# Performance work log

Measured on AMD Instinct MI355X. Metric: run time of the kernel, lower is better.

Reference implementation:

```python
import jax, jax.numpy as jnp
import numpy as np

N_KERNELS = 5
MUL_FACTOR = 2.0
# 2.0 ** (arange(5) - 2) = [0.25, 0.5, 1, 2, 4]
BANDWIDTH_MULTIPLIERS = MUL_FACTOR ** (np.arange(N_KERNELS) - N_KERNELS // 2)


def setup_inputs() -> dict:
    key = jax.random.key(0)
    kx, ky = jax.random.split(key)
    X = jax.random.normal(kx, (4096, 256), dtype=jnp.float32)
    Y = jax.random.normal(ky, (4096, 256), dtype=jnp.float32)
    return {"X": X, "Y": Y}


def _pairwise_sq_dists(Z):
    # ||z_i - z_j||^2 via GEMM; clamp tiny negatives from roundoff.
    sq = jnp.sum(Z * Z, axis=-1)  # [2N]
    d2 = sq[:, None] + sq[None, :] - 2.0 * (Z @ Z.T)  # [2N, 2N]
    return jnp.maximum(d2, 0.0)


def reference(X, Y):
    n = X.shape[0]
    Z = jnp.concatenate([X, Y], axis=0)  # [2N, D]
    d2 = _pairwise_sq_dists(Z)  # [2N, 2N]
    n_samples = d2.shape[0]
    # bandwidth uses .data in torch -> detached
    bandwidth = jax.lax.stop_gradient(d2.sum()) / (n_samples ** 2 - n_samples)
    mults = jnp.asarray(BANDWIDTH_MULTIPLIERS, dtype=d2.dtype)  # [5]
    # K = sum_k exp(-d2 / (bandwidth * mult_k))
    K = jnp.exp(-d2[None, :, :] / (bandwidth * mults)[:, None, None]).sum(axis=0)
    XX = K[:n, :n].mean()
    XY = K[:n, n:].mean()
    YY = K[n:, n:].mean()
    return XX - 2.0 * XY + YY
```

## Files before the change

### kernel.cpp

```cpp
#include <hip/hip_runtime.h>
#include <math.h>


#define N_HALF 4096
#define DIM 256
#define M_TOT 8192
#define TILE 128
#define NT 64
#define NT_HALF 32
#define NCHUNK 512

typedef unsigned short ushort_t;
typedef __attribute__((ext_vector_type(8))) short short8;
typedef __attribute__((ext_vector_type(4))) float floatx4;

__device__ ushort_t g_zf[M_TOT * DIM];

__device__ __forceinline__ ushort_t f2bf(float f) {
    unsigned u = __float_as_uint(f);
    u += 0x7fffu + ((u >> 16) & 1u);
    return (ushort_t)(u >> 16);
}

__device__ __forceinline__ void gload_lds16(const ushort_t* g, ushort_t* l) {
    __builtin_amdgcn_global_load_lds(
        (const __attribute__((address_space(1))) void*)g,
        (__attribute__((address_space(3))) void*)l, 16, 0, 0);
}

__device__ __forceinline__ void stage_slice2(const ushort_t* gA, const ushort_t* gB,
                                             ushort_t* buf, int kk0,
                                             int wave, int lane) {
#pragma unroll
    for (int s = 0; s < 2; ++s) {
#pragma unroll
        for (int i = 0; i < 2; ++i) {
            const int c = wave * 2 + i;
            gload_lds16(gA + (size_t)c * 4096 + (kk0 + s) * 512 + lane * 8,
                        buf + s * 4096 + c * 512);
            gload_lds16(gB + (size_t)c * 4096 + (kk0 + s) * 512 + lane * 8,
                        buf + 8192 + s * 4096 + c * 512);
        }
    }
}

__device__ __forceinline__ void compute_kk(const ushort_t* lA, const ushort_t* lB,
                                           int a0, int b0, int laneoff,
                                           floatx4 (&accv)[4][4]) {
    short8 af[4], bf[4];
#pragma unroll
    for (int mi = 0; mi < 4; ++mi)
        af[mi] = *(const short8*)(lA + (a0 + mi) * 512 + laneoff);
#pragma unroll
    for (int ni = 0; ni < 4; ++ni)
        bf[ni] = *(const short8*)(lB + (b0 + ni) * 512 + laneoff);
#pragma unroll
    for (int mi = 0; mi < 4; ++mi)
#pragma unroll
        for (int ni = 0; ni < 4; ++ni)
            accv[mi][ni] = __builtin_amdgcn_mfma_f32_16x16x32_bf16(
                af[mi], bf[ni], accv[mi][ni], 0, 0, 0);
}

__global__ __launch_bounds__(256) void k_prep(const float* __restrict__ X,
                                              const float* __restrict__ Y,
                                              float* __restrict__ sq,
                                              float* __restrict__ colsum_r,
                                              float* __restrict__ Ssum_r) {
    __shared__ float cpart[4][256];
    __shared__ float spart[4];
    const int t = threadIdx.x, wave = t >> 6, lane = t & 63;
    const int row0 = blockIdx.x * 16 + wave * 4;
    const int kk = lane >> 3, q = (lane >> 1) & 3, j0 = (lane & 1) * 4;
    float c0 = 0.f, c1 = 0.f, c2 = 0.f, c3 = 0.f, ssum = 0.f;
#pragma unroll
    for (int i = 0; i < 4; ++i) {
        const int row = row0 + i;
        const float* p = (row < N_HALF) ? (X + (size_t)row * DIM)
                                        : (Y + (size_t)(row - N_HALF) * DIM);
        const float4 v = *((const float4*)p + lane);
        ushort4 hi;
        hi.x = f2bf(v.x); hi.y = f2bf(v.y); hi.z = f2bf(v.z); hi.w = f2bf(v.w);
        const int rb = row >> 4, m = row & 15;
        *(ushort4*)(g_zf + (size_t)rb * 4096 + kk * 512 + q * 128 + m * 8 + j0) = hi;
        c0 += v.x; c1 += v.y; c2 += v.z; c3 += v.w;
        float s = fmaf(v.x, v.x, fmaf(v.y, v.y, fmaf(v.z, v.z, v.w * v.w)));
#pragma unroll
        for (int off = 32; off > 0; off >>= 1) s += __shfl_xor(s, off);
        if (lane == 0) sq[row] = s;
        ssum += s;
    }
    float4 cp; cp.x = c0; cp.y = c1; cp.z = c2; cp.w = c3;
    *(float4*)&cpart[wave][lane * 4] = cp;
    if (lane == 0) spart[wave] = ssum;
    __syncthreads();
    const float cs = cpart[0][t] + cpart[1][t] + cpart[2][t] + cpart[3][t];
    const int rep = blockIdx.x & 7;
    atomicAdd(&colsum_r[rep * 256 + t], cs);
    if (t == 0) atomicAdd(&Ssum_r[rep], spart[0] + spart[1] + spart[2] + spart[3]);
}

__global__ __launch_bounds__(256) void k_bw(const float* __restrict__ colsum_r,
                                            const float* __restrict__ Ssum_r,
                                            float* __restrict__ c2out) {
    __shared__ double sred[4];
    const int t = threadIdx.x, lane = t & 63, wave = t >> 6;
    float csf = 0.f;
#pragma unroll
    for (int r = 0; r < 8; ++r) csf += colsum_r[r * 256 + t];
    double p = (double)csf * (double)csf;
#pragma unroll
    for (int off = 32; off > 0; off >>= 1) p += __shfl_xor(p, off);
    if (lane == 0) sred[wave] = p;
    __syncthreads();
    if (t == 0) {
        const double SS = sred[0] + sred[1] + sred[2] + sred[3];
        float Sf = 0.f;
#pragma unroll
        for (int r = 0; r < 8; ++r) Sf += Ssum_r[r];
        const double sum_d2 = 2.0 * (double)M_TOT * (double)Sf - 2.0 * SS;
        const double bw = sum_d2 / ((double)M_TOT * (double)M_TOT - (double)M_TOT);
        c2out[0] = (float)(1.4426950408889634 / (4.0 * bw));
    }
}

__global__ __launch_bounds__(256, 2) void k_gram(const float* __restrict__ sq,
                                                 const float* __restrict__ c2p,
                                                 double* __restrict__ acc,
                                                 unsigned* __restrict__ cnt,
                                                 float* __restrict__ out) {
    __shared__ __attribute__((aligned(16))) ushort_t lds[2][16384];
    __shared__ double redw[4][3];

    const int bid = (int)blockIdx.x;
    const int cc = (bid & 7) * 64 + (bid >> 3);
    const int nst = ((cc & 15) == 0) ? 5 : 4;
    const int f0 = cc * 4 + ((cc + 15) >> 4);

    const int t = threadIdx.x;
    const int lane = t & 63, wave = t >> 6;
    const int l15 = lane & 15, quad = lane >> 4;
    const int wrow = (wave >> 1) * 64, wcol = (wave & 1) * 64;
    const int a0 = (wave >> 1) * 4, b0 = (wave & 1) * 4;
    const int laneoff = quad * 128 + l15 * 8;

    const float c2 = c2p[0];
    const float twoc2 = 2.f * c2;

    int ti = (int)((129.0f - sqrtf(16641.0f - 8.0f * (float)f0)) * 0.5f);
    if (ti < 0) ti = 0; if (ti > NT - 1) ti = NT - 1;
    while (ti * NT - ti * (ti - 1) / 2 > f0) --ti;
    while ((ti + 1) * NT - (ti + 1) * ti / 2 <= f0) ++ti;
    int tj = ti + (f0 - (ti * NT - ti * (ti - 1) / 2));

    const ushort_t* cgA = g_zf + (size_t)ti * 8 * 4096;
    const ushort_t* cgB = g_zf + (size_t)tj * 8 * 4096;

    stage_slice2(cgA, cgB, lds[0], 0, wave, lane);
    __syncthreads();

    double lxx = 0.0, lxy = 0.0, lyy = 0.0;
    int cur = 0;

#pragma unroll 1
    for (int s = 0; s < nst; ++s) {
        int nti = ti, ntj = tj + 1;
        if (ntj == NT) { ++nti; ntj = nti; }
        const ushort_t* ngA = g_zf + (size_t)nti * 8 * 4096;
        const ushort_t* ngB = g_zf + (size_t)ntj * 8 * 4096;

        floatx4 accv[4][4];
#pragma unroll
        for (int mi = 0; mi < 4; ++mi)
#pragma unroll
            for (int ni = 0; ni < 4; ++ni) accv[mi][ni] = (floatx4)0.f;

#pragma unroll
        for (int kk2 = 0; kk2 < 4; ++kk2) {
            if (kk2 < 3)
                stage_slice2(cgA, cgB, lds[cur ^ 1], (kk2 + 1) * 2, wave, lane);
            else if (s < nst - 1)
                stage_slice2(ngA, ngB, lds[cur ^ 1], 0, wave, lane);
            compute_kk(lds[cur], lds[cur] + 8192, a0, b0, laneoff, accv);
            compute_kk(lds[cur] + 4096, lds[cur] + 8192 + 4096,
                       a0, b0, laneoff, accv);
            __syncthreads();
            cur ^= 1;
        }

        const int arow0 = ti * TILE, brow0 = tj * TILE;
        float nsj[4];
#pragma unroll
        for (int ni = 0; ni < 4; ++ni)
            nsj[ni] = -c2 * sq[brow0 + wcol + ni * 16 + l15];
        floatx4 nsi4[4];
#pragma unroll
        for (int mi = 0; mi < 4; ++mi) {
            const float4 sv = *(const float4*)&sq[arow0 + wrow + mi * 16 + quad * 4];
            nsi4[mi][0] = -c2 * sv.x; nsi4[mi][1] = -c2 * sv.y;
            nsi4[mi][2] = -c2 * sv.z; nsi4[mi][3] = -c2 * sv.w;
        }
        floatx4 sum4 = (floatx4)0.f;
#pragma unroll
        for (int mi = 0; mi < 4; ++mi) {
#pragma unroll
            for (int ni = 0; ni < 4; ++ni) {
                const floatx4 addv = nsi4[mi] + (floatx4)nsj[ni];
                floatx4 arg = twoc2 * accv[mi][ni] + addv;
                floatx4 tt;
#pragma unroll
                for (int r = 0; r < 4; ++r) tt[r] = exp2f(fminf(arg[r], 0.f));
                const floatx4 t2 = tt * tt, t4 = t2 * t2, t8 = t4 * t4, t16 = t8 * t8;
                sum4 += (tt + t2) + (t4 + t8) + t16;
            }
        }
        const float fsum = (sum4[0] + sum4[1]) + (sum4[2] + sum4[3]);
        const double contrib = ((ti == tj) ? 1.0 : 2.0) * (double)fsum;
        if (tj < NT_HALF)       lxx += contrib;
        else if (ti < NT_HALF)  lxy += contrib;
        else                    lyy += contrib;

        ti = nti; tj = ntj; cgA = ngA; cgB = ngB;
    }

#pragma unroll
    for (int off = 32; off > 0; off >>= 1) {
        lxx += __shfl_xor(lxx, off);
        lxy += __shfl_xor(lxy, off);
        lyy += __shfl_xor(lyy, off);
    }
    if (lane == 0) { redw[wave][0] = lxx; redw[wave][1] = lxy; redw[wave][2] = lyy; }
    __syncthreads();
    if (t == 0) {
        double sxx = 0.0, sxy = 0.0, syy = 0.0;
#pragma unroll
        for (int wv = 0; wv < 4; ++wv) {
            sxx += redw[wv][0]; sxy += redw[wv][1]; syy += redw[wv][2];
        }
        if (sxx != 0.0) atomicAdd(&acc[0], sxx);
        if (sxy != 0.0) atomicAdd(&acc[1], sxy);
        if (syy != 0.0) atomicAdd(&acc[2], syy);
        __threadfence();
        const unsigned old = atomicAdd(cnt, 1u);
        if (old == (0xAAAAAAAAu + (unsigned)(NCHUNK - 1)) ||
            old == (unsigned)(NCHUNK - 1)) {
            const double xx = atomicAdd(&acc[0], 0.0);
            const double xy = atomicAdd(&acc[1], 0.0);
            const double yy = atomicAdd(&acc[2], 0.0);
            out[0] = (float)((xx + yy - xy) *
                             (1.0 / ((double)N_HALF * (double)N_HALF)));
        }
    }
}

extern "C" void kernel_launch(void* const* d_in, const int* in_sizes, int n_in,
                              void* d_out, int out_size, void* d_ws, size_t ws_size,
                              hipStream_t stream) {
    const float* X = (const float*)d_in[0];
    const float* Y = (const float*)d_in[1];
    char* ws = (char*)d_ws;
    float* sq        = (float*)ws;
    float* colsum_r  = (float*)(ws + 32768);
    float* Ssum_r    = (float*)(ws + 40960);
    unsigned* cnt    = (unsigned*)(ws + 40992);
    double* acc      = (double*)(ws + 41000);
    float* c2ws      = (float*)(ws + 41024);
    float* out = (float*)d_out;

    hipLaunchKernelGGL(k_prep, dim3(512), dim3(256), 0, stream,
                       X, Y, sq, colsum_r, Ssum_r);
    hipLaunchKernelGGL(k_bw, dim3(1), dim3(256), 0, stream,
                       colsum_r, Ssum_r, c2ws);
    hipLaunchKernelGGL(k_gram, dim3(NCHUNK), dim3(256), 0, stream,
                       sq, c2ws, acc, cnt, out);
}
```

Before: 115.5 us.

## Deepen GEMM staging to 4-buffer ring with explicit vmcnt waits

Replaces the double-buffered LDS staging of two k-slices per step with a four-slot ring holding single k-slices, keeping three slices in flight ahead of compute. A single barrier per slice is now gated by explicit s_waitcnt vmcnt counts instead of a full __syncthreads. Fragment loads are issued before the next global-to-LDS prefetch, and the MFMA block runs with raised wave priority. The goal is to hide global load latency across tile boundaries and cut barrier stalls. The cost is hand-tuned wait counts that must exactly match the number of outstanding loads.

```diff
diff --git a/kernel.cpp b/kernel.cpp
--- a/kernel.cpp
+++ b/kernel.cpp
@@ -28,38 +28,14 @@
         (__attribute__((address_space(3))) void*)l, 16, 0, 0);
 }
 
-__device__ __forceinline__ void stage_slice2(const ushort_t* gA, const ushort_t* gB,
-                                             ushort_t* buf, int kk0,
-                                             int wave, int lane) {
-#pragma unroll
-    for (int s = 0; s < 2; ++s) {
-#pragma unroll
-        for (int i = 0; i < 2; ++i) {
-            const int c = wave * 2 + i;
-            gload_lds16(gA + (size_t)c * 4096 + (kk0 + s) * 512 + lane * 8,
-                        buf + s * 4096 + c * 512);
-            gload_lds16(gB + (size_t)c * 4096 + (kk0 + s) * 512 + lane * 8,
-                        buf + 8192 + s * 4096 + c * 512);
-        }
-    }
-}
-
-__device__ __forceinline__ void compute_kk(const ushort_t* lA, const ushort_t* lB,
-                                           int a0, int b0, int laneoff,
-                                           floatx4 (&accv)[4][4]) {
-    short8 af[4], bf[4];
-#pragma unroll
-    for (int mi = 0; mi < 4; ++mi)
-        af[mi] = *(const short8*)(lA + (a0 + mi) * 512 + laneoff);
-#pragma unroll
-    for (int ni = 0; ni < 4; ++ni)
-        bf[ni] = *(const short8*)(lB + (b0 + ni) * 512 + laneoff);
-#pragma unroll
-    for (int mi = 0; mi < 4; ++mi)
-#pragma unroll
-        for (int ni = 0; ni < 4; ++ni)
-            accv[mi][ni] = __builtin_amdgcn_mfma_f32_16x16x32_bf16(
-                af[mi], bf[ni], accv[mi][ni], 0, 0, 0);
+__device__ __forceinline__ void stage1(const ushort_t* gA, const ushort_t* gB,
+                                       int kk, ushort_t* buf, int wave, int lane) {
+#pragma unroll
+    for (int i = 0; i < 2; ++i) {
+        const int c = wave * 2 + i;
+        gload_lds16(gA + (size_t)c * 4096 + kk * 512 + lane * 8, buf + c * 512);
+        gload_lds16(gB + (size_t)c * 4096 + kk * 512 + lane * 8, buf + 4096 + c * 512);
+    }
 }
 
 __global__ __launch_bounds__(256) void k_prep(const float* __restrict__ X,
@@ -129,7 +105,7 @@
                                                  double* __restrict__ acc,
                                                  unsigned* __restrict__ cnt,
                                                  float* __restrict__ out) {
-    __shared__ __attribute__((aligned(16))) ushort_t lds[2][16384];
+    __shared__ __attribute__((aligned(16))) ushort_t lds[4][8192];
     __shared__ double redw[4][3];
 
     const int bid = (int)blockIdx.x;
@@ -153,21 +129,25 @@
     while ((ti + 1) * NT - (ti + 1) * ti / 2 <= f0) ++ti;
     int tj = ti + (f0 - (ti * NT - ti * (ti - 1) / 2));
 
-    const ushort_t* cgA = g_zf + (size_t)ti * 8 * 4096;
-    const ushort_t* cgB = g_zf + (size_t)tj * 8 * 4096;
-
-    stage_slice2(cgA, cgB, lds[0], 0, wave, lane);
-    __syncthreads();
+    int s_ti = ti, s_tj = tj, s_kk = 0;
+    const ushort_t* sgA = g_zf + (size_t)s_ti * 32768;
+    const ushort_t* sgB = g_zf + (size_t)s_tj * 32768;
+#define ADV_STAGE() do { if (++s_kk == 8) { s_kk = 0; ++s_tj;                 \
+        if (s_tj == NT) { ++s_ti; s_tj = s_ti; }                              \
+        sgA = g_zf + (size_t)s_ti * 32768;                                    \
+        sgB = g_zf + (size_t)s_tj * 32768; } } while (0)
+
+#pragma unroll
+    for (int p = 0; p < 3; ++p) {
+        stage1(sgA, sgB, s_kk, lds[p], wave, lane);
+        ADV_STAGE();
+    }
 
     double lxx = 0.0, lxy = 0.0, lyy = 0.0;
-    int cur = 0;
 
 #pragma unroll 1
     for (int s = 0; s < nst; ++s) {
-        int nti = ti, ntj = tj + 1;
-        if (ntj == NT) { ++nti; ntj = nti; }
-        const ushort_t* ngA = g_zf + (size_t)nti * 8 * 4096;
-        const ushort_t* ngB = g_zf + (size_t)ntj * 8 * 4096;
+        const bool last = (s == nst - 1);
 
         floatx4 accv[4][4];
 #pragma unroll
@@ -176,16 +156,36 @@
             for (int ni = 0; ni < 4; ++ni) accv[mi][ni] = (floatx4)0.f;
 
 #pragma unroll
-        for (int kk2 = 0; kk2 < 4; ++kk2) {
-            if (kk2 < 3)
-                stage_slice2(cgA, cgB, lds[cur ^ 1], (kk2 + 1) * 2, wave, lane);
-            else if (s < nst - 1)
-                stage_slice2(ngA, ngB, lds[cur ^ 1], 0, wave, lane);
-            compute_kk(lds[cur], lds[cur] + 8192, a0, b0, laneoff, accv);
-            compute_kk(lds[cur] + 4096, lds[cur] + 8192 + 4096,
-                       a0, b0, laneoff, accv);
-            __syncthreads();
-            cur ^= 1;
+        for (int kkc = 0; kkc < 8; ++kkc) {
+            if (last && kkc == 6)      asm volatile("s_waitcnt vmcnt(4)" ::: "memory");
+            else if (last && kkc == 7) asm volatile("s_waitcnt vmcnt(0)" ::: "memory");
+            else                       asm volatile("s_waitcnt vmcnt(8)" ::: "memory");
+            __builtin_amdgcn_s_barrier();
+            __builtin_amdgcn_sched_barrier(0);
+
+            const ushort_t* lA = lds[kkc & 3];
+            const ushort_t* lB = lds[kkc & 3] + 4096;
+            short8 af[4], bf[4];
+#pragma unroll
+            for (int mi = 0; mi < 4; ++mi)
+                af[mi] = *(const short8*)(lA + (a0 + mi) * 512 + laneoff);
+#pragma unroll
+            for (int ni = 0; ni < 4; ++ni)
+                bf[ni] = *(const short8*)(lB + (b0 + ni) * 512 + laneoff);
+
+            if (!last || kkc < 5) {
+                stage1(sgA, sgB, s_kk, lds[(kkc + 3) & 3], wave, lane);
+                ADV_STAGE();
+            }
+
+            __builtin_amdgcn_s_setprio(1);
+#pragma unroll
+            for (int mi = 0; mi < 4; ++mi)
+#pragma unroll
+                for (int ni = 0; ni < 4; ++ni)
+                    accv[mi][ni] = __builtin_amdgcn_mfma_f32_16x16x32_bf16(
+                        af[mi], bf[ni], accv[mi][ni], 0, 0, 0);
+            __builtin_amdgcn_s_setprio(0);
         }
 
         const int arow0 = ti * TILE, brow0 = tj * TILE;
@@ -220,8 +220,9 @@
         else if (ti < NT_HALF)  lxy += contrib;
         else                    lyy += contrib;
 
-        ti = nti; tj = ntj; cgA = ngA; cgB = ngB;
-    }
+        ++tj; if (tj == NT) { ++ti; tj = ti; }
+    }
+#undef ADV_STAGE
 
 #pragma unroll
     for (int off = 32; off > 0; off >>= 1) {
```

Measured after the change: 113.8 us. Within noise of the previous version (-1.5%).

## Load MFMA fragments directly from global memory with register pipelining, drop LDS staging

Applied to the files above, without the earlier changes.

Removes the LDS double-buffer and global_load_lds staging in the Gram kernel. Each wave now reads its bf16 MFMA fragments straight from global memory into registers, prefetching three k-slices ahead in a software pipeline that also carries into the next tile. This drops the per-slice __syncthreads barriers and LDS traffic. In exchange, operands shared between waves are fetched redundantly from global/L2, and the kernel holds many more VGPRs for the in-flight fragments.

```diff
diff --git a/kernel.cpp b/kernel.cpp
--- a/kernel.cpp
+++ b/kernel.cpp
@@ -20,46 +20,6 @@
     unsigned u = __float_as_uint(f);
     u += 0x7fffu + ((u >> 16) & 1u);
     return (ushort_t)(u >> 16);
-}
-
-__device__ __forceinline__ void gload_lds16(const ushort_t* g, ushort_t* l) {
-    __builtin_amdgcn_global_load_lds(
-        (const __attribute__((address_space(1))) void*)g,
-        (__attribute__((address_space(3))) void*)l, 16, 0, 0);
-}
-
-__device__ __forceinline__ void stage_slice2(const ushort_t* gA, const ushort_t* gB,
-                                             ushort_t* buf, int kk0,
-                                             int wave, int lane) {
-#pragma unroll
-    for (int s = 0; s < 2; ++s) {
-#pragma unroll
-        for (int i = 0; i < 2; ++i) {
-            const int c = wave * 2 + i;
-            gload_lds16(gA + (size_t)c * 4096 + (kk0 + s) * 512 + lane * 8,
-                        buf + s * 4096 + c * 512);
-            gload_lds16(gB + (size_t)c * 4096 + (kk0 + s) * 512 + lane * 8,
-                        buf + 8192 + s * 4096 + c * 512);
-        }
-    }
-}
-
-__device__ __forceinline__ void compute_kk(const ushort_t* lA, const ushort_t* lB,
-                                           int a0, int b0, int laneoff,
-                                           floatx4 (&accv)[4][4]) {
-    short8 af[4], bf[4];
-#pragma unroll
-    for (int mi = 0; mi < 4; ++mi)
-        af[mi] = *(const short8*)(lA + (a0 + mi) * 512 + laneoff);
-#pragma unroll
-    for (int ni = 0; ni < 4; ++ni)
-        bf[ni] = *(const short8*)(lB + (b0 + ni) * 512 + laneoff);
-#pragma unroll
-    for (int mi = 0; mi < 4; ++mi)
-#pragma unroll
-        for (int ni = 0; ni < 4; ++ni)
-            accv[mi][ni] = __builtin_amdgcn_mfma_f32_16x16x32_bf16(
-                af[mi], bf[ni], accv[mi][ni], 0, 0, 0);
 }
 
 __global__ __launch_bounds__(256) void k_prep(const float* __restrict__ X,
@@ -124,12 +84,31 @@
     }
 }
 
+#define LOADSET(AF, BF, pA, pB, KK)                                           \
+    do {                                                                      \
+        _Pragma("unroll")                                                     \
+        for (int mi_ = 0; mi_ < 4; ++mi_)                                     \
+            AF[mi_] = *(const short8*)((pA) + (size_t)mi_ * 4096 + (KK) * 512);\
+        _Pragma("unroll")                                                     \
+        for (int ni_ = 0; ni_ < 4; ++ni_)                                     \
+            BF[ni_] = *(const short8*)((pB) + (size_t)ni_ * 4096 + (KK) * 512);\
+    } while (0)
+
+#define MFMASET(AF, BF)                                                       \
+    do {                                                                      \
+        _Pragma("unroll")                                                     \
+        for (int mi_ = 0; mi_ < 4; ++mi_)                                     \
+            _Pragma("unroll")                                                 \
+            for (int ni_ = 0; ni_ < 4; ++ni_)                                 \
+                accv[mi_][ni_] = __builtin_amdgcn_mfma_f32_16x16x32_bf16(     \
+                    AF[mi_], BF[ni_], accv[mi_][ni_], 0, 0, 0);               \
+    } while (0)
+
 __global__ __launch_bounds__(256, 2) void k_gram(const float* __restrict__ sq,
                                                  const float* __restrict__ c2p,
                                                  double* __restrict__ acc,
                                                  unsigned* __restrict__ cnt,
                                                  float* __restrict__ out) {
-    __shared__ __attribute__((aligned(16))) ushort_t lds[2][16384];
     __shared__ double redw[4][3];
 
     const int bid = (int)blockIdx.x;
@@ -153,21 +132,25 @@
     while ((ti + 1) * NT - (ti + 1) * ti / 2 <= f0) ++ti;
     int tj = ti + (f0 - (ti * NT - ti * (ti - 1) / 2));
 
-    const ushort_t* cgA = g_zf + (size_t)ti * 8 * 4096;
-    const ushort_t* cgB = g_zf + (size_t)tj * 8 * 4096;
-
-    stage_slice2(cgA, cgB, lds[0], 0, wave, lane);
-    __syncthreads();
+    const ushort_t* cA = g_zf + (size_t)(ti * 8 + a0) * 4096 + laneoff;
+    const ushort_t* cB = g_zf + (size_t)(tj * 8 + b0) * 4096 + laneoff;
+
+    short8 af0[4], bf0[4], af1[4], bf1[4], af2[4], bf2[4], af3[4], bf3[4];
+
+    LOADSET(af0, bf0, cA, cB, 0);
+    LOADSET(af1, bf1, cA, cB, 1);
+    LOADSET(af2, bf2, cA, cB, 2);
 
     double lxx = 0.0, lxy = 0.0, lyy = 0.0;
-    int cur = 0;
 
 #pragma unroll 1
     for (int s = 0; s < nst; ++s) {
+        const bool notlast = (s < nst - 1);
+
         int nti = ti, ntj = tj + 1;
         if (ntj == NT) { ++nti; ntj = nti; }
-        const ushort_t* ngA = g_zf + (size_t)nti * 8 * 4096;
-        const ushort_t* ngB = g_zf + (size_t)ntj * 8 * 4096;
+        const ushort_t* nA = g_zf + (size_t)(nti * 8 + a0) * 4096 + laneoff;
+        const ushort_t* nB = g_zf + (size_t)(ntj * 8 + b0) * 4096 + laneoff;
 
         floatx4 accv[4][4];
 #pragma unroll
@@ -175,18 +158,14 @@
 #pragma unroll
             for (int ni = 0; ni < 4; ++ni) accv[mi][ni] = (floatx4)0.f;
 
-#pragma unroll
-        for (int kk2 = 0; kk2 < 4; ++kk2) {
-            if (kk2 < 3)
-                stage_slice2(cgA, cgB, lds[cur ^ 1], (kk2 + 1) * 2, wave, lane);
-            else if (s < nst - 1)
-                stage_slice2(ngA, ngB, lds[cur ^ 1], 0, wave, lane);
-            compute_kk(lds[cur], lds[cur] + 8192, a0, b0, laneoff, accv);
-            compute_kk(lds[cur] + 4096, lds[cur] + 8192 + 4096,
-                       a0, b0, laneoff, accv);
-            __syncthreads();
-            cur ^= 1;
-        }
+         LOADSET(af3, bf3, cA, cB, 3);              MFMASET(af0, bf0);
+         LOADSET(af0, bf0, cA, cB, 4);              MFMASET(af1, bf1);
+         LOADSET(af1, bf1, cA, cB, 5);              MFMASET(af2, bf2);
+         LOADSET(af2, bf2, cA, cB, 6);              MFMASET(af3, bf3);
+         LOADSET(af3, bf3, cA, cB, 7);              MFMASET(af0, bf0);
+         if (notlast) LOADSET(af0, bf0, nA, nB, 0); MFMASET(af1, bf1);
+         if (notlast) LOADSET(af1, bf1, nA, nB, 1); MFMASET(af2, bf2);
+         if (notlast) LOADSET(af2, bf2, nA, nB, 2); MFMASET(af3, bf3);
 
         const int arow0 = ti * TILE, brow0 = tj * TILE;
         float nsj[4];
@@ -220,7 +199,7 @@
         else if (ti < NT_HALF)  lxy += contrib;
         else                    lyy += contrib;
 
-        ti = nti; tj = ntj; cgA = ngA; cgB = ngB;
+        ti = nti; tj = ntj; cA = nA; cB = nB;
     }
 
 #pragma unroll
```

Result: faster. 112.9 us (-2.3%).
